# Kernel optimization log

Hardware: AMD Instinct MI355X
Metric: run time of the kernel (lower is better)

Reference implementation:

```python
import jax, jax.numpy as jnp
import numpy as np

L, DIRS, FEAT, H, B, T = 2, 2, 512, 256, 64, 1024  # layers, directions, feat_dim, per-dir hidden, n_trees, chain_len


def setup_inputs() -> dict:
    key = jax.random.key(0)
    ks = jax.random.split(key, 4)
    s = 0.05
    features = jax.random.normal(ks[0], (B, T, FEAT), jnp.float32)
    Wx = jax.random.normal(ks[1], (L, DIRS, FEAT, 5 * H), jnp.float32) * s
    bx = jnp.zeros((L, DIRS, 5 * H), jnp.float32)
    Wh = jax.random.normal(ks[2], (L, DIRS, H, 5 * H), jnp.float32) * s
    # forget-gate bias slice [2H:3H] initialized to 1.0 as in ChainLSTM
    bh = jnp.zeros((L, DIRS, 5 * H), jnp.float32).at[:, :, 2 * H:3 * H].set(1.0)
    Wp = jax.random.normal(ks[3], (L, DIRS, FEAT, H), jnp.float32) * s
    bp = jnp.zeros((L, DIRS, H), jnp.float32)
    return dict(features=features, Wx=Wx, bx=bx, Wh=Wh, bh=bh, Wp=Wp, bp=bp)


def _run_direction(x, Wx_d, bx_d, Wh_d, bh_d, Wp_d, bp_d, reverse):
    # x: [T, B, F]. Precompute input projections as one big GEMM (memory-bound stream),
    # then scan only carries the tiny [B,H] @ [H,5H] recurrence.
    gx = x @ Wx_d + bx_d          # [T, B, 5H]
    px = x @ Wp_d + bp_d          # [T, B, H] highway projection

    def step(carry, inp):
        c, h = carry
        g, p = inp
        z = g + h @ Wh_d + bh_d
        i, o, f, u, r = jnp.split(z, 5, axis=-1)
        c = jax.nn.sigmoid(i) * jnp.tanh(u) + jax.nn.sigmoid(f) * c
        hh = jax.nn.sigmoid(o) * jnp.tanh(c)
        rg = jax.nn.sigmoid(r)
        hf = rg * hh + (1.0 - rg) * p  # highway gate
        return (c, hf), hf

    zero = jnp.zeros((x.shape[1], bh_d.shape[-1] // 5), x.dtype)
    _, hs = jax.lax.scan(step, (zero, zero), (gx, px), reverse=reverse)
    return hs  # [T, B, H], aligned to original node positions


def reference(features, Wx, bx, Wh, bh, Wp, bp):
    x = jnp.swapaxes(features, 0, 1)  # [T, B, F]
    n_layers = Wx.shape[0]
    for l in range(n_layers):
        outs = []
        for d in range(Wx.shape[1]):  # 0 = foreward, 1 = backward
            hs = _run_direction(x, Wx[l, d], bx[l, d], Wh[l, d], bh[l, d],
                                Wp[l, d], bp[l, d], reverse=(d == 1))
            outs.append(hs)
        x = jnp.concatenate(outs, axis=-1)  # [T, B, 2H] -> next layer input
    return jnp.swapaxes(x, 0, 1)  # [B, T, 2H]
```

## Files before the change

### kernel.cpp

```cpp
#include <hip/hip_runtime.h>
#include <hip/hip_bf16.h>

#define LAYERS 2
#define DIRS   2
#define FEAT   512
#define HDIM   256
#define BATCH  64
#define TLEN   1024
#define FIVEH  1280
#define CHUNK  64
#define NCHUNK (TLEN / CHUNK)
#define NW     8

typedef short bf16x8 __attribute__((ext_vector_type(8)));
typedef float f32x4  __attribute__((ext_vector_type(4)));

__device__ __forceinline__ unsigned short f2bf(float x) {
    unsigned u = __float_as_uint(x);
    unsigned r = (u + 0x7fffu + ((u >> 16) & 1u)) >> 16;
    return (unsigned short)r;
}
__device__ __forceinline__ float bf2f(unsigned short h) {
    return __uint_as_float(((unsigned)h) << 16);
}
__device__ __forceinline__ float sigf(float x) {
    return 1.0f / (1.0f + __expf(-x));
}
__device__ __forceinline__ float tanhfast(float x) {
    return 1.0f - 2.0f / (__expf(2.0f * x) + 1.0f);
}

__global__ __launch_bounds__(256) void castT_kernel(
    const float* __restrict__ src, unsigned short* __restrict__ dst, int K, int N)
{
    __shared__ float tile[32][33];
    const int n0 = blockIdx.x * 32, k0 = blockIdx.y * 32;
    const size_t slab = (size_t)blockIdx.z * K * N;
    src += slab; dst += slab;
    const int tx = threadIdx.x & 31, ty = threadIdx.x >> 5;
    #pragma unroll
    for (int r = 0; r < 32; r += 8)
        tile[ty + r][tx] = src[(size_t)(k0 + ty + r) * N + (n0 + tx)];
    __syncthreads();
    #pragma unroll
    for (int r = 0; r < 32; r += 8)
        dst[(size_t)(n0 + ty + r) * K + (k0 + tx)] = f2bf(tile[tx][ty + r]);
}

__global__ __launch_bounds__(64) void init_kernel(int* __restrict__ flags) {
    if (threadIdx.x < 2 * NW) flags[threadIdx.x * 16] = 0;
}

__global__ __launch_bounds__(256) void proj_kernel(
    const float* __restrict__ features,
    const unsigned short* __restrict__ x1,
    const unsigned short* __restrict__ Wx_t,
    const unsigned short* __restrict__ Wp_t,
    const float* __restrict__ bx, const float* __restrict__ bh,
    const float* __restrict__ bp,
    unsigned short* __restrict__ gx_c,
    unsigned short* __restrict__ px_c,
    int layer, int chunk)
{
    const int ntb = blockIdx.x;
    const int mt  = blockIdx.y;
    const int d   = blockIdx.z;
    const int tid = threadIdx.x;
    const int wave = tid >> 6, lane = tid & 63;

    __shared__ __align__(16) unsigned short Alds[64][40];
    __shared__ __align__(16) unsigned short Blds[64][40];

    const int n0 = ntb * 64;
    const bool isWx = (n0 < FIVEH);
    const unsigned short* Wt = isWx
        ? (Wx_t + ((size_t)(layer * 2 + d) * FIVEH + n0) * FEAT)
        : (Wp_t + ((size_t)(layer * 2 + d) * HDIM + (n0 - FIVEH)) * FEAT);

    const int m0 = mt * 64;
    const int lm = tid >> 2;
    const int lkb = tid & 3;

    const int mrow = m0 + lm;
    const int tl = mrow >> 6;
    const int b  = mrow & 63;
    const int tglob = (d == 0) ? (chunk * CHUNK + tl) : (TLEN - 1 - (chunk * CHUNK + tl));
    const float* Arow0 = features + ((size_t)b * TLEN + tglob) * FEAT;
    const unsigned short* Arow1 = x1 + ((size_t)tglob * BATCH + b) * FEAT;

    f32x4 acc[4];
    #pragma unroll
    for (int i = 0; i < 4; ++i) acc[i] = 0.0f;

    const int fr = lane & 15, quad = lane >> 4;

    for (int k0 = 0; k0 < FEAT; k0 += 32) {
        if (layer == 0) {
            float4 a0 = *(const float4*)(Arow0 + k0 + lkb * 8);
            float4 a1 = *(const float4*)(Arow0 + k0 + lkb * 8 + 4);
            unsigned short* dst = &Alds[lm][lkb * 8];
            dst[0] = f2bf(a0.x); dst[1] = f2bf(a0.y);
            dst[2] = f2bf(a0.z); dst[3] = f2bf(a0.w);
            dst[4] = f2bf(a1.x); dst[5] = f2bf(a1.y);
            dst[6] = f2bf(a1.z); dst[7] = f2bf(a1.w);
        } else {
            uint4 a = *(const uint4*)(Arow1 + k0 + lkb * 8);
            *(uint4*)&Alds[lm][lkb * 8] = a;
        }
        uint4 bv = *(const uint4*)(Wt + (size_t)lm * FEAT + k0 + lkb * 8);
        *(uint4*)&Blds[lm][lkb * 8] = bv;
        __syncthreads();

        bf16x8 af = *(const bf16x8*)&Alds[wave * 16 + fr][quad * 8];
        #pragma unroll
        for (int nt = 0; nt < 4; ++nt) {
            bf16x8 bf = *(const bf16x8*)&Blds[nt * 16 + fr][quad * 8];
            acc[nt] = __builtin_amdgcn_mfma_f32_16x16x32_bf16(af, bf, acc[nt], 0, 0, 0);
        }
        __syncthreads();
    }

    const int ldoff = layer * 2 + d;
    #pragma unroll
    for (int nt = 0; nt < 4; ++nt) {
        const int n = n0 + nt * 16 + fr;
        #pragma unroll
        for (int r = 0; r < 4; ++r) {
            const int m2 = m0 + wave * 16 + quad * 4 + r;
            const int tl2 = m2 >> 6, b2 = m2 & 63;
            float v = acc[nt][r];
            if (n < FIVEH) {
                v += bx[(size_t)ldoff * FIVEH + n] + bh[(size_t)ldoff * FIVEH + n];
                const int g = n >> 8, j = n & 255;
                gx_c[((((size_t)d * CHUNK + tl2) * 5 + g) * HDIM + j) * BATCH + b2] = f2bf(v);
            } else {
                const int j = n - FIVEH;
                v += bp[(size_t)ldoff * HDIM + j];
                px_c[(((size_t)d * CHUNK + tl2) * HDIM + j) * BATCH + b2] = f2bf(v);
            }
        }
    }
}

__global__ __launch_bounds__(256, 1) void recur_kernel(
    const unsigned short* __restrict__ gx_c,
    const unsigned short* __restrict__ px_c,
    const unsigned short* __restrict__ Wh_t,
    unsigned short* __restrict__ x1,
    float* __restrict__ out,
    float* __restrict__ cbuf,
    unsigned short* __restrict__ hbuf,
    int* __restrict__ flags,
    int layer, int chunk)
{
    const int blk = blockIdx.x;
    const int d = blk >> 3, wg = blk & 7;
    const int tid = threadIdx.x;
    const int wave = tid >> 6, lane = tid & 63;
    const int mw = wave >> 1, jh = wave & 1;
    const int col = lane & 15, quad = lane >> 4;
    const int jg = wg * 32 + jh * 16 + col;

    bf16x8 bfr[5][8];
    const unsigned short* Wb = Wh_t + (size_t)(layer * 2 + d) * FIVEH * HDIM;
    #pragma unroll
    for (int g = 0; g < 5; ++g)
        #pragma unroll
        for (int ks = 0; ks < 8; ++ks)
            bfr[g][ks] = *(const bf16x8*)(Wb + (size_t)(g * HDIM + jg) * HDIM + ks * 32 + quad * 8);

    float cst[2][4];
    #pragma unroll
    for (int mt = 0; mt < 2; ++mt)
        #pragma unroll
        for (int r = 0; r < 4; ++r) {
            const int b = (2 * mw + mt) * 16 + quad * 4 + r;
            cst[mt][r] = (chunk == 0) ? 0.0f
                       : cbuf[((size_t)d * BATCH + b) * HDIM + jg];
        }

    const int base = layer * TLEN + chunk * CHUNK;
    int* myflag = &flags[(d * NW + wg) * 16];

    for (int s = 0; s < CHUNK; ++s) {
        const int gs = base + s;

        if (tid < NW) {
            while (__hip_atomic_load(&flags[(d * NW + tid) * 16],
                                     __ATOMIC_RELAXED, __HIP_MEMORY_SCOPE_AGENT) < gs) { }
        }
        __syncthreads();
        __threadfence();

        f32x4 acc[2][5];
        #pragma unroll
        for (int mt = 0; mt < 2; ++mt)
            #pragma unroll
            for (int g = 0; g < 5; ++g) acc[mt][g] = 0.0f;

        if ((gs & (TLEN - 1)) != 0) {
            const unsigned short* hs = hbuf + (size_t)(((gs + 1) & 1) * 2 + d) * BATCH * HDIM;
            bf16x8 af[2][8];
            #pragma unroll
            for (int mt = 0; mt < 2; ++mt)
                #pragma unroll
                for (int ks = 0; ks < 8; ++ks)
                    af[mt][ks] = *(const bf16x8*)(hs + (size_t)((2 * mw + mt) * 16 + col) * HDIM
                                                  + ks * 32 + quad * 8);
            #pragma unroll
            for (int ks = 0; ks < 8; ++ks)
                #pragma unroll
                for (int g = 0; g < 5; ++g) {
                    acc[0][g] = __builtin_amdgcn_mfma_f32_16x16x32_bf16(af[0][ks], bfr[g][ks], acc[0][g], 0, 0, 0);
                    acc[1][g] = __builtin_amdgcn_mfma_f32_16x16x32_bf16(af[1][ks], bfr[g][ks], acc[1][g], 0, 0, 0);
                }
        }

        ushort4 gxv[2][5], pxv[2];
        #pragma unroll
        for (int mt = 0; mt < 2; ++mt) {
            const size_t bb = (2 * mw + mt) * 16 + quad * 4;
            #pragma unroll
            for (int g = 0; g < 5; ++g)
                gxv[mt][g] = *(const ushort4*)(gx_c + ((((size_t)d * CHUNK + s) * 5 + g) * HDIM + jg) * BATCH + bb);
            pxv[mt] = *(const ushort4*)(px_c + (((size_t)d * CHUNK + s) * HDIM + jg) * BATCH + bb);
        }

        const int tpos = chunk * CHUNK + s;
        const int tglob = d ? (TLEN - 1 - tpos) : tpos;
        unsigned short* hdst = hbuf + (size_t)((gs & 1) * 2 + d) * BATCH * HDIM;

        #pragma unroll
        for (int mt = 0; mt < 2; ++mt) {
            const unsigned short* gq0 = (const unsigned short*)&gxv[mt][0];
            const unsigned short* gq1 = (const unsigned short*)&gxv[mt][1];
            const unsigned short* gq2 = (const unsigned short*)&gxv[mt][2];
            const unsigned short* gq3 = (const unsigned short*)&gxv[mt][3];
            const unsigned short* gq4 = (const unsigned short*)&gxv[mt][4];
            const unsigned short* pq  = (const unsigned short*)&pxv[mt];
            #pragma unroll
            for (int r = 0; r < 4; ++r) {
                const float z0 = acc[mt][0][r] + bf2f(gq0[r]);
                const float z1 = acc[mt][1][r] + bf2f(gq1[r]);
                const float z2 = acc[mt][2][r] + bf2f(gq2[r]);
                const float z3 = acc[mt][3][r] + bf2f(gq3[r]);
                const float z4 = acc[mt][4][r] + bf2f(gq4[r]);
                const float p  = bf2f(pq[r]);
                const float ig = sigf(z0);
                const float og = sigf(z1);
                const float fg = sigf(z2);
                const float ug = tanhfast(z3);
                const float rg = sigf(z4);
                const float cc = ig * ug + fg * cst[mt][r];
                cst[mt][r] = cc;
                const float hh = og * tanhfast(cc);
                const float h = rg * hh + (1.0f - rg) * p;
                const int b = (2 * mw + mt) * 16 + quad * 4 + r;
                hdst[(size_t)b * HDIM + jg] = f2bf(h);
                if (layer == 0)
                    x1[((size_t)tglob * BATCH + b) * 512 + d * HDIM + jg] = f2bf(h);
                else
                    out[((size_t)b * TLEN + tglob) * 512 + d * HDIM + jg] = h;
            }
        }

        __syncthreads();
        if (tid == 0) {
            __threadfence();
            __hip_atomic_store(myflag, gs + 1, __ATOMIC_RELAXED, __HIP_MEMORY_SCOPE_AGENT);
        }
    }

    #pragma unroll
    for (int mt = 0; mt < 2; ++mt)
        #pragma unroll
        for (int r = 0; r < 4; ++r) {
            const int b = (2 * mw + mt) * 16 + quad * 4 + r;
            cbuf[((size_t)d * BATCH + b) * HDIM + jg] = cst[mt][r];
        }
}

extern "C" void kernel_launch(void* const* d_in, const int* in_sizes, int n_in,
                              void* d_out, int out_size, void* d_ws, size_t ws_size,
                              hipStream_t stream) {
    const float* features = (const float*)d_in[0];
    const float* Wx = (const float*)d_in[1];
    const float* bx = (const float*)d_in[2];
    const float* Wh = (const float*)d_in[3];
    const float* bh = (const float*)d_in[4];
    const float* Wp = (const float*)d_in[5];
    const float* bp = (const float*)d_in[6];
    float* out = (float*)d_out;

    char* ws = (char*)d_ws;
    size_t off = 0;
    auto alloc = [&](size_t bytes) -> void* {
        void* p = ws + off;
        off += (bytes + 255) & ~(size_t)255;
        return p;
    };
    unsigned short* Wx_t = (unsigned short*)alloc((size_t)LAYERS * DIRS * FIVEH * FEAT * 2);
    unsigned short* Wh_t = (unsigned short*)alloc((size_t)LAYERS * DIRS * FIVEH * HDIM * 2);
    unsigned short* Wp_t = (unsigned short*)alloc((size_t)LAYERS * DIRS * HDIM * FEAT * 2);
    unsigned short* x1   = (unsigned short*)alloc((size_t)TLEN * BATCH * 512 * 2);
    unsigned short* gx_c = (unsigned short*)alloc((size_t)DIRS * CHUNK * BATCH * FIVEH * 2);
    unsigned short* px_c = (unsigned short*)alloc((size_t)DIRS * CHUNK * BATCH * HDIM * 2);
    float* cbuf = (float*)alloc((size_t)DIRS * BATCH * HDIM * 4);
    unsigned short* hbuf = (unsigned short*)alloc((size_t)2 * DIRS * BATCH * HDIM * 2);
    int* flags = (int*)alloc((size_t)2 * NW * 16 * 4);

    init_kernel<<<1, 64, 0, stream>>>(flags);
    castT_kernel<<<dim3(FIVEH / 32, FEAT / 32, 4), 256, 0, stream>>>(Wx, Wx_t, FEAT, FIVEH);
    castT_kernel<<<dim3(FIVEH / 32, HDIM / 32, 4), 256, 0, stream>>>(Wh, Wh_t, HDIM, FIVEH);
    castT_kernel<<<dim3(HDIM / 32, FEAT / 32, 4), 256, 0, stream>>>(Wp, Wp_t, FEAT, HDIM);

    for (int l = 0; l < LAYERS; ++l) {
        for (int c = 0; c < NCHUNK; ++c) {
            proj_kernel<<<dim3(24, 64, 2), 256, 0, stream>>>(
                features, x1, Wx_t, Wp_t, bx, bh, bp, gx_c, px_c, l, c);
            recur_kernel<<<DIRS * NW, 256, 0, stream>>>(
                gx_c, px_c, Wh_t, x1, out, cbuf, hbuf, flags, l, c);
        }
    }
}
```

Measured before the change: 17.61 ms.

## Halve recurrence workgroups, use shared counter barrier and LDS-staged hidden exchange

Each direction's recurrence now runs on 4 workgroups instead of 8. Each wave covers all 64 batch rows for 16 hidden columns. The per-workgroup flag array with its polling threads is replaced by one atomic counter per direction, polled with s_sleep. The gx/px loads are issued before the wait so they overlap the barrier. The previous hidden state is loaded into padded LDS once per step and shared across waves, and the new h is staged in LDS and written back as 64-bit atomic stores. The cost being attacked is inter-workgroup synchronisation latency and redundant global reads of h, paid for with more MFMA work per workgroup and two extra __syncthreads per step.

```diff
diff --git a/kernel.cpp b/kernel.cpp
--- a/kernel.cpp
+++ b/kernel.cpp
@@ -10,7 +10,9 @@
 #define FIVEH  1280
 #define CHUNK  64
 #define NCHUNK (TLEN / CHUNK)
-#define NW     8
+#define NW     4
+#define HSTR   296
+#define TSTR   68
 
 typedef short bf16x8 __attribute__((ext_vector_type(8)));
 typedef float f32x4  __attribute__((ext_vector_type(4)));
@@ -47,8 +49,8 @@
         dst[(size_t)(n0 + ty + r) * K + (k0 + tx)] = f2bf(tile[tx][ty + r]);
 }
 
-__global__ __launch_bounds__(64) void init_kernel(int* __restrict__ flags) {
-    if (threadIdx.x < 2 * NW) flags[threadIdx.x * 16] = 0;
+__global__ __launch_bounds__(64) void init_kernel(int* __restrict__ cnt) {
+    if (threadIdx.x < DIRS) cnt[threadIdx.x * 16] = 0;
 }
 
 __global__ __launch_bounds__(256) void proj_kernel(
@@ -149,17 +151,20 @@
     unsigned short* __restrict__ x1,
     float* __restrict__ out,
     float* __restrict__ cbuf,
-    unsigned short* __restrict__ hbuf,
-    int* __restrict__ flags,
+    unsigned long long* __restrict__ hbuf,
+    int* __restrict__ cnt,
     int layer, int chunk)
 {
     const int blk = blockIdx.x;
-    const int d = blk >> 3, wg = blk & 7;
+    const int d = blk >> 2, wg = blk & 3;
     const int tid = threadIdx.x;
     const int wave = tid >> 6, lane = tid & 63;
-    const int mw = wave >> 1, jh = wave & 1;
     const int col = lane & 15, quad = lane >> 4;
-    const int jg = wg * 32 + jh * 16 + col;
+    const int wgj0 = wg * 64;
+    const int jg = wgj0 + wave * 16 + col;
+
+    __shared__ __align__(16) unsigned short Hs[64 * HSTR];
+    __shared__ __align__(16) unsigned short Ht[64 * TSTR];
 
     bf16x8 bfr[5][8];
     const unsigned short* Wb = Wh_t + (size_t)(layer * 2 + d) * FIVEH * HDIM;
@@ -169,69 +174,74 @@
         for (int ks = 0; ks < 8; ++ks)
             bfr[g][ks] = *(const bf16x8*)(Wb + (size_t)(g * HDIM + jg) * HDIM + ks * 32 + quad * 8);
 
-    float cst[2][4];
-    #pragma unroll
-    for (int mt = 0; mt < 2; ++mt)
+    float cst[4][4];
+    #pragma unroll
+    for (int mt = 0; mt < 4; ++mt)
         #pragma unroll
         for (int r = 0; r < 4; ++r) {
-            const int b = (2 * mw + mt) * 16 + quad * 4 + r;
+            const int b = mt * 16 + quad * 4 + r;
             cst[mt][r] = (chunk == 0) ? 0.0f
                        : cbuf[((size_t)d * BATCH + b) * HDIM + jg];
         }
 
     const int base = layer * TLEN + chunk * CHUNK;
-    int* myflag = &flags[(d * NW + wg) * 16];
+    int* cptr = cnt + d * 16;
 
     for (int s = 0; s < CHUNK; ++s) {
         const int gs = base + s;
 
-        if (tid < NW) {
-            while (__hip_atomic_load(&flags[(d * NW + tid) * 16],
-                                     __ATOMIC_RELAXED, __HIP_MEMORY_SCOPE_AGENT) < gs) { }
-        }
-        __syncthreads();
-        __threadfence();
-
-        f32x4 acc[2][5];
-        #pragma unroll
-        for (int mt = 0; mt < 2; ++mt)
-            #pragma unroll
-            for (int g = 0; g < 5; ++g) acc[mt][g] = 0.0f;
-
-        if ((gs & (TLEN - 1)) != 0) {
-            const unsigned short* hs = hbuf + (size_t)(((gs + 1) & 1) * 2 + d) * BATCH * HDIM;
-            bf16x8 af[2][8];
-            #pragma unroll
-            for (int mt = 0; mt < 2; ++mt)
-                #pragma unroll
-                for (int ks = 0; ks < 8; ++ks)
-                    af[mt][ks] = *(const bf16x8*)(hs + (size_t)((2 * mw + mt) * 16 + col) * HDIM
-                                                  + ks * 32 + quad * 8);
-            #pragma unroll
-            for (int ks = 0; ks < 8; ++ks)
-                #pragma unroll
-                for (int g = 0; g < 5; ++g) {
-                    acc[0][g] = __builtin_amdgcn_mfma_f32_16x16x32_bf16(af[0][ks], bfr[g][ks], acc[0][g], 0, 0, 0);
-                    acc[1][g] = __builtin_amdgcn_mfma_f32_16x16x32_bf16(af[1][ks], bfr[g][ks], acc[1][g], 0, 0, 0);
-                }
-        }
-
-        ushort4 gxv[2][5], pxv[2];
-        #pragma unroll
-        for (int mt = 0; mt < 2; ++mt) {
-            const size_t bb = (2 * mw + mt) * 16 + quad * 4;
+        ushort4 gxv[4][5], pxv[4];
+        #pragma unroll
+        for (int mt = 0; mt < 4; ++mt) {
+            const size_t bb = mt * 16 + quad * 4;
             #pragma unroll
             for (int g = 0; g < 5; ++g)
                 gxv[mt][g] = *(const ushort4*)(gx_c + ((((size_t)d * CHUNK + s) * 5 + g) * HDIM + jg) * BATCH + bb);
             pxv[mt] = *(const ushort4*)(px_c + (((size_t)d * CHUNK + s) * HDIM + jg) * BATCH + bb);
         }
 
-        const int tpos = chunk * CHUNK + s;
-        const int tglob = d ? (TLEN - 1 - tpos) : tpos;
-        unsigned short* hdst = hbuf + (size_t)((gs & 1) * 2 + d) * BATCH * HDIM;
-
-        #pragma unroll
-        for (int mt = 0; mt < 2; ++mt) {
+        if (gs > 0) {
+            const int target = NW * gs;
+            while (__hip_atomic_load(cptr, __ATOMIC_RELAXED, __HIP_MEMORY_SCOPE_AGENT) < target)
+                __builtin_amdgcn_s_sleep(1);
+        }
+
+        f32x4 acc[4][5];
+        #pragma unroll
+        for (int mt = 0; mt < 4; ++mt)
+            #pragma unroll
+            for (int g = 0; g < 5; ++g) acc[mt][g] = 0.0f;
+
+        if ((gs & (TLEN - 1)) != 0) {
+            const unsigned long long* hsrc =
+                hbuf + (size_t)(((gs + 1) & 1) * 2 + d) * BATCH * 64;
+            #pragma unroll
+            for (int ii = 0; ii < 16; ++ii) {
+                const int idx = tid + 256 * ii;
+                const int b = idx >> 6, j4 = idx & 63;
+                unsigned long long v = __hip_atomic_load(hsrc + (size_t)b * 64 + j4,
+                                                         __ATOMIC_RELAXED, __HIP_MEMORY_SCOPE_AGENT);
+                *(unsigned long long*)&Hs[b * HSTR + j4 * 4] = v;
+            }
+            __syncthreads();
+
+            #pragma unroll
+            for (int ks = 0; ks < 8; ++ks) {
+                bf16x8 af[4];
+                #pragma unroll
+                for (int mt = 0; mt < 4; ++mt)
+                    af[mt] = *(const bf16x8*)&Hs[(mt * 16 + col) * HSTR + ks * 32 + quad * 8];
+                #pragma unroll
+                for (int mt = 0; mt < 4; ++mt)
+                    #pragma unroll
+                    for (int g = 0; g < 5; ++g)
+                        acc[mt][g] = __builtin_amdgcn_mfma_f32_16x16x32_bf16(af[mt], bfr[g][ks], acc[mt][g], 0, 0, 0);
+            }
+        }
+
+        float hv[4][4];
+        #pragma unroll
+        for (int mt = 0; mt < 4; ++mt) {
             const unsigned short* gq0 = (const unsigned short*)&gxv[mt][0];
             const unsigned short* gq1 = (const unsigned short*)&gxv[mt][1];
             const unsigned short* gq2 = (const unsigned short*)&gxv[mt][2];
@@ -255,27 +265,45 @@
                 cst[mt][r] = cc;
                 const float hh = og * tanhfast(cc);
                 const float h = rg * hh + (1.0f - rg) * p;
-                const int b = (2 * mw + mt) * 16 + quad * 4 + r;
-                hdst[(size_t)b * HDIM + jg] = f2bf(h);
+                hv[mt][r] = h;
+                const int b = mt * 16 + quad * 4 + r;
+                Ht[b * TSTR + wave * 16 + col] = f2bf(h);
+            }
+        }
+        __syncthreads();
+
+        unsigned long long* hdst = hbuf + (size_t)((gs & 1) * 2 + d) * BATCH * 64;
+        #pragma unroll
+        for (int ii = 0; ii < 4; ++ii) {
+            const int idx = tid + 256 * ii;
+            const int b = idx >> 4, jq = idx & 15;
+            const unsigned long long v = *(const unsigned long long*)&Ht[b * TSTR + jq * 4];
+            __hip_atomic_store(hdst + (size_t)b * 64 + (wgj0 >> 2) + jq, v,
+                               __ATOMIC_RELAXED, __HIP_MEMORY_SCOPE_AGENT);
+        }
+        __syncthreads();
+        if (tid == 0)
+            __hip_atomic_fetch_add(cptr, 1, __ATOMIC_RELAXED, __HIP_MEMORY_SCOPE_AGENT);
+
+        const int tpos = chunk * CHUNK + s;
+        const int tglob = d ? (TLEN - 1 - tpos) : tpos;
+        #pragma unroll
+        for (int mt = 0; mt < 4; ++mt)
+            #pragma unroll
+            for (int r = 0; r < 4; ++r) {
+                const int b = mt * 16 + quad * 4 + r;
                 if (layer == 0)
-                    x1[((size_t)tglob * BATCH + b) * 512 + d * HDIM + jg] = f2bf(h);
+                    x1[((size_t)tglob * BATCH + b) * 512 + d * HDIM + jg] = f2bf(hv[mt][r]);
                 else
-                    out[((size_t)b * TLEN + tglob) * 512 + d * HDIM + jg] = h;
-            }
-        }
-
-        __syncthreads();
-        if (tid == 0) {
-            __threadfence();
-            __hip_atomic_store(myflag, gs + 1, __ATOMIC_RELAXED, __HIP_MEMORY_SCOPE_AGENT);
-        }
+                    out[((size_t)b * TLEN + tglob) * 512 + d * HDIM + jg] = hv[mt][r];
+            }
     }
 
     #pragma unroll
-    for (int mt = 0; mt < 2; ++mt)
+    for (int mt = 0; mt < 4; ++mt)
         #pragma unroll
         for (int r = 0; r < 4; ++r) {
-            const int b = (2 * mw + mt) * 16 + quad * 4 + r;
+            const int b = mt * 16 + quad * 4 + r;
             cbuf[((size_t)d * BATCH + b) * HDIM + jg] = cst[mt][r];
         }
 }
@@ -306,10 +334,10 @@
     unsigned short* gx_c = (unsigned short*)alloc((size_t)DIRS * CHUNK * BATCH * FIVEH * 2);
     unsigned short* px_c = (unsigned short*)alloc((size_t)DIRS * CHUNK * BATCH * HDIM * 2);
     float* cbuf = (float*)alloc((size_t)DIRS * BATCH * HDIM * 4);
-    unsigned short* hbuf = (unsigned short*)alloc((size_t)2 * DIRS * BATCH * HDIM * 2);
-    int* flags = (int*)alloc((size_t)2 * NW * 16 * 4);
-
-    init_kernel<<<1, 64, 0, stream>>>(flags);
+    unsigned long long* hbuf = (unsigned long long*)alloc((size_t)2 * DIRS * BATCH * 64 * 8);
+    int* cnt = (int*)alloc((size_t)DIRS * 16 * 4);
+
+    init_kernel<<<1, 64, 0, stream>>>(cnt);
     castT_kernel<<<dim3(FIVEH / 32, FEAT / 32, 4), 256, 0, stream>>>(Wx, Wx_t, FEAT, FIVEH);
     castT_kernel<<<dim3(FIVEH / 32, HDIM / 32, 4), 256, 0, stream>>>(Wh, Wh_t, HDIM, FIVEH);
     castT_kernel<<<dim3(HDIM / 32, FEAT / 32, 4), 256, 0, stream>>>(Wp, Wp_t, FEAT, HDIM);
@@ -319,7 +347,7 @@
             proj_kernel<<<dim3(24, 64, 2), 256, 0, stream>>>(
                 features, x1, Wx_t, Wp_t, bx, bh, bp, gx_c, px_c, l, c);
             recur_kernel<<<DIRS * NW, 256, 0, stream>>>(
-                gx_c, px_c, Wh_t, x1, out, cbuf, hbuf, flags, l, c);
+                gx_c, px_c, Wh_t, x1, out, cbuf, hbuf, cnt, l, c);
         }
     }
 }
```

Result: slower. 29.20 ms (+65.8%).
